# Kernel tuning notes

Measured on AMD Instinct MI355X. Metric: run time of the kernel, lower is better.

The kernel has to match this reference:

```python
import jax, jax.numpy as jnp
import numpy as np

MARGIN = 0.3


def setup_inputs() -> dict:
    key = jax.random.key(0)
    k1, k2 = jax.random.split(key)
    B, D, NCLS = 4096, 2048, 64
    inputs = jax.random.normal(k1, (B, D), dtype=jnp.float32)
    targets = jax.random.randint(k2, (B,), 0, NCLS, dtype=jnp.int64)
    return {"inputs": inputs, "targets": targets}


def _triplet_loss(inputs, targets, margin):
    sq = jnp.sum(inputs * inputs, axis=1)  # [B]
    distmat = sq[:, None] + sq[None, :] - 2.0 * (inputs @ inputs.T)  # [B, B]
    distmat = jnp.sqrt(jnp.clip(distmat, 1e-12, None))
    same = targets[None, :] == targets[:, None]  # [B, B]; includes diagonal
    neg_inf = jnp.float32(-jnp.inf)
    pos_inf = jnp.float32(jnp.inf)
    d_pos = jnp.max(jnp.where(same, distmat, neg_inf), axis=1)  # hardest positive
    d_neg = jnp.min(jnp.where(same, pos_inf, distmat), axis=1)  # hardest negative
    # MarginRankingLoss(x1=d_neg, x2=d_pos, y=1): mean(relu(-(d_neg - d_pos) + margin))
    return jnp.mean(jax.nn.relu(d_pos - d_neg + margin))


def reference(inputs, targets):
    return _triplet_loss(inputs, targets, MARGIN)
```

## Files before the change

kernel.cpp:

```cpp
#include <hip/hip_runtime.h>
#include <hip/hip_bf16.h>


typedef __attribute__((ext_vector_type(8))) short short8;
typedef __attribute__((ext_vector_type(4))) float f32x4;
using bf16 = __hip_bfloat16;

#define BN_ROWS 4096
#define D_DIM   2048
#define TILE    128
#define BK      64
#define MARGIN  0.3f

__device__ __forceinline__ void gload16(const bf16* g, bf16* l) {
  __builtin_amdgcn_global_load_lds(
      (const __attribute__((address_space(1))) void*)g,
      (__attribute__((address_space(3))) void*)l, 16, 0, 0);
}

__global__ __launch_bounds__(256) void prep_kernel(
    const float* __restrict__ x, bf16* __restrict__ xb, float* __restrict__ sqv,
    unsigned* __restrict__ pos, unsigned* __restrict__ neg) {
  const int row = blockIdx.x;
  const int t = threadIdx.x;
  const float4* xr = (const float4*)(x + (size_t)row * D_DIM) + (size_t)t * 2;
  float4 a = xr[0];
  float4 b = xr[1];
  float s = a.x * a.x + a.y * a.y + a.z * a.z + a.w * a.w +
            b.x * b.x + b.y * b.y + b.z * b.z + b.w * b.w;
  union { short8 v; bf16 h[8]; } u;
  u.h[0] = __float2bfloat16(a.x);
  u.h[1] = __float2bfloat16(a.y);
  u.h[2] = __float2bfloat16(a.z);
  u.h[3] = __float2bfloat16(a.w);
  u.h[4] = __float2bfloat16(b.x);
  u.h[5] = __float2bfloat16(b.y);
  u.h[6] = __float2bfloat16(b.z);
  u.h[7] = __float2bfloat16(b.w);
  *(short8*)(xb + (size_t)row * D_DIM + (size_t)t * 8) = u.v;

  #pragma unroll
  for (int o = 32; o; o >>= 1) s += __shfl_down(s, o, 64);
  __shared__ float red[4];
  if ((t & 63) == 0) red[t >> 6] = s;
  __syncthreads();
  if (t == 0) {
    sqv[row] = red[0] + red[1] + red[2] + red[3];
    pos[row] = 0u;
    neg[row] = 0x7F800000u;
  }
}

__global__ __launch_bounds__(256) void gram_kernel(
    const bf16* __restrict__ xb, const float* __restrict__ sqv,
    const int* __restrict__ tgt, unsigned* __restrict__ pos,
    unsigned* __restrict__ neg) {
  __shared__ bf16 As[TILE * BK];
  __shared__ bf16 Bs[TILE * BK];
  const int t = threadIdx.x;
  const int wave = t >> 6, lane = t & 63;
  const int rowBase = blockIdx.y * TILE;
  const int colBase = blockIdx.x * TILE;
  const int wr = wave >> 1, wc = wave & 1;
  const int lhi = lane >> 4, llo = lane & 15;

  f32x4 acc[4][4];
  #pragma unroll
  for (int m = 0; m < 4; ++m)
    #pragma unroll
    for (int n = 0; n < 4; ++n) acc[m][n] = (f32x4){0.f, 0.f, 0.f, 0.f};

  const int srow = lane >> 3;
  const int swz = (lane & 7) ^ srow;

  for (int k0 = 0; k0 < D_DIM; k0 += BK) {
    #pragma unroll
    for (int c = 0; c < 4; ++c) {
      const int chunk = wave * 4 + c;
      const size_t kcol = (size_t)k0 + (size_t)swz * 8;
      gload16(xb + (size_t)(rowBase + chunk * 8 + srow) * D_DIM + kcol,
              As + chunk * 512);
      gload16(xb + (size_t)(colBase + chunk * 8 + srow) * D_DIM + kcol,
              Bs + chunk * 512);
    }
    asm volatile("s_waitcnt vmcnt(0)" ::: "memory");
    __syncthreads();

    #pragma unroll
    for (int kk = 0; kk < 2; ++kk) {
      short8 af[4], bfr[4];
      #pragma unroll
      for (int m = 0; m < 4; ++m) {
        const int row = wr * 64 + m * 16 + llo;
        const int c16 = (kk * 4 + lhi) ^ (row & 7);
        af[m] = *(const short8*)(As + row * 64 + c16 * 8);
      }
      #pragma unroll
      for (int n = 0; n < 4; ++n) {
        const int row = wc * 64 + n * 16 + llo;
        const int c16 = (kk * 4 + lhi) ^ (row & 7);
        bfr[n] = *(const short8*)(Bs + row * 64 + c16 * 8);
      }
      #pragma unroll
      for (int m = 0; m < 4; ++m)
        #pragma unroll
        for (int n = 0; n < 4; ++n)
          acc[m][n] = __builtin_amdgcn_mfma_f32_16x16x32_bf16(
              af[m], bfr[n], acc[m][n], 0, 0, 0);
    }
    __syncthreads();
  }

  float sqj[4];
  int tgj[4];
  #pragma unroll
  for (int n = 0; n < 4; ++n) {
    const int j = colBase + wc * 64 + n * 16 + llo;
    sqj[n] = sqv[j];
    tgj[n] = tgt[j];
  }
  #pragma unroll
  for (int m = 0; m < 4; ++m) {
    #pragma unroll
    for (int r = 0; r < 4; ++r) {
      const int i = rowBase + wr * 64 + m * 16 + lhi * 4 + r;
      const float sqi = sqv[i];
      const int tgi = tgt[i];
      float pm = 0.0f;
      float nm = __uint_as_float(0x7F800000u);
      #pragma unroll
      for (int n = 0; n < 4; ++n) {
        const float g = acc[m][n][r];
        const float d2 = sqi + sqj[n] - 2.0f * g;
        const float d = sqrtf(fmaxf(d2, 1e-12f));
        if (tgj[n] == tgi) pm = fmaxf(pm, d);
        else               nm = fminf(nm, d);
      }
      #pragma unroll
      for (int o = 1; o < 16; o <<= 1) {
        pm = fmaxf(pm, __shfl_xor(pm, o, 64));
        nm = fminf(nm, __shfl_xor(nm, o, 64));
      }
      if (llo == 0) {
        atomicMax(pos + i, __float_as_uint(pm));
        atomicMin(neg + i, __float_as_uint(nm));
      }
    }
  }
}

__global__ __launch_bounds__(1024) void loss_kernel(
    const unsigned* __restrict__ pos, const unsigned* __restrict__ neg,
    float* __restrict__ out) {
  const int t = threadIdx.x;
  float s = 0.f;
  for (int i = t; i < BN_ROWS; i += 1024) {
    const float dp = __uint_as_float(pos[i]);
    const float dn = __uint_as_float(neg[i]);
    const float v = dp - dn + MARGIN;
    s += v > 0.f ? v : 0.f;
  }
  #pragma unroll
  for (int o = 32; o; o >>= 1) s += __shfl_down(s, o, 64);
  __shared__ float red[16];
  if ((t & 63) == 0) red[t >> 6] = s;
  __syncthreads();
  if (t < 16) {
    float v = red[t];
    #pragma unroll
    for (int o = 8; o; o >>= 1) v += __shfl_down(v, o, 16);
    if (t == 0) out[0] = v * (1.0f / (float)BN_ROWS);
  }
}

extern "C" void kernel_launch(void* const* d_in, const int* in_sizes, int n_in,
                              void* d_out, int out_size, void* d_ws, size_t ws_size,
                              hipStream_t stream) {
  const float* x = (const float*)d_in[0];
  const int* tgt = (const int*)d_in[1];
  float* out = (float*)d_out;

  char* ws = (char*)d_ws;
  bf16* xb = (bf16*)ws;
  float* sqv = (float*)(ws + (size_t)BN_ROWS * D_DIM * 2);
  unsigned* pos = (unsigned*)((char*)sqv + BN_ROWS * 4);
  unsigned* neg = (unsigned*)((char*)pos + BN_ROWS * 4);

  prep_kernel<<<BN_ROWS, 256, 0, stream>>>(x, xb, sqv, pos, neg);
  gram_kernel<<<dim3(BN_ROWS / TILE, BN_ROWS / TILE), 256, 0, stream>>>(
      xb, sqv, tgt, pos, neg);
  loss_kernel<<<1, 1024, 0, stream>>>(pos, neg, out);
}
```

Measured before the change: 173.2 us.

## Exploit Gram matrix symmetry by computing only upper-triangular tiles

The gram kernel now launches only the upper-triangular 128x128 tiles, mapping a linear block id to (row, col) tile indices. Each tile reduces its distances both per row and per column, with atomics on both, so the mirrored tile is never computed. This roughly halves the MFMA and load work but adds column reductions, extra atomics and index math. The prep kernel also switches to coalesced float4 loads with 8-byte bf16 stores.

New measurement: 173.3 us. About the same (+0.1%).

```diff
diff --git a/kernel.cpp b/kernel.cpp
--- a/kernel.cpp
+++ b/kernel.cpp
@@ -10,6 +10,8 @@
 #define D_DIM   2048
 #define TILE    128
 #define BK      64
+#define NB      (BN_ROWS / TILE)
+#define NBLK    (NB * (NB + 1) / 2)
 #define MARGIN  0.3f
 
 __device__ __forceinline__ void gload16(const bf16* g, bf16* l) {
@@ -23,22 +25,21 @@
     unsigned* __restrict__ pos, unsigned* __restrict__ neg) {
   const int row = blockIdx.x;
   const int t = threadIdx.x;
-  const float4* xr = (const float4*)(x + (size_t)row * D_DIM) + (size_t)t * 2;
-  float4 a = xr[0];
-  float4 b = xr[1];
-  float s = a.x * a.x + a.y * a.y + a.z * a.z + a.w * a.w +
-            b.x * b.x + b.y * b.y + b.z * b.z + b.w * b.w;
-  union { short8 v; bf16 h[8]; } u;
-  u.h[0] = __float2bfloat16(a.x);
-  u.h[1] = __float2bfloat16(a.y);
-  u.h[2] = __float2bfloat16(a.z);
-  u.h[3] = __float2bfloat16(a.w);
-  u.h[4] = __float2bfloat16(b.x);
-  u.h[5] = __float2bfloat16(b.y);
-  u.h[6] = __float2bfloat16(b.z);
-  u.h[7] = __float2bfloat16(b.w);
-  *(short8*)(xb + (size_t)row * D_DIM + (size_t)t * 8) = u.v;
-
+  const float4* xr = (const float4*)(x + (size_t)row * D_DIM);
+  bf16* xbr = xb + (size_t)row * D_DIM;
+  float s = 0.f;
+  #pragma unroll
+  for (int p = 0; p < 2; ++p) {
+    const int idx = t + p * 256;
+    float4 a = xr[idx];
+    s += a.x * a.x + a.y * a.y + a.z * a.z + a.w * a.w;
+    union { ushort4 v; bf16 h[4]; } u;
+    u.h[0] = __float2bfloat16(a.x);
+    u.h[1] = __float2bfloat16(a.y);
+    u.h[2] = __float2bfloat16(a.z);
+    u.h[3] = __float2bfloat16(a.w);
+    *(ushort4*)(xbr + (size_t)idx * 4) = u.v;
+  }
   #pragma unroll
   for (int o = 32; o; o >>= 1) s += __shfl_down(s, o, 64);
   __shared__ float red[4];
@@ -59,8 +60,15 @@
   __shared__ bf16 Bs[TILE * BK];
   const int t = threadIdx.x;
   const int wave = t >> 6, lane = t & 63;
-  const int rowBase = blockIdx.y * TILE;
-  const int colBase = blockIdx.x * TILE;
+
+  const int id = blockIdx.x;
+  int by = (int)(0.5f * (65.0f - sqrtf(4225.0f - 8.0f * (float)id)));
+  while (by * NB - (by * (by - 1)) / 2 > id) --by;
+  while ((by + 1) * NB - ((by + 1) * by) / 2 <= id) ++by;
+  const int bx = by + (id - (by * NB - (by * (by - 1)) / 2));
+  const int rowBase = by * TILE;
+  const int colBase = bx * TILE;
+
   const int wr = wave >> 1, wc = wave & 1;
   const int lhi = lane >> 4, llo = lane & 15;
 
@@ -111,6 +119,7 @@
     __syncthreads();
   }
 
+  const float inf = __uint_as_float(0x7F800000u);
   float sqj[4];
   int tgj[4];
   #pragma unroll
@@ -119,6 +128,9 @@
     sqj[n] = sqv[j];
     tgj[n] = tgt[j];
   }
+  float colP[4] = {0.f, 0.f, 0.f, 0.f};
+  float colN[4] = {inf, inf, inf, inf};
+
   #pragma unroll
   for (int m = 0; m < 4; ++m) {
     #pragma unroll
@@ -126,15 +138,19 @@
       const int i = rowBase + wr * 64 + m * 16 + lhi * 4 + r;
       const float sqi = sqv[i];
       const int tgi = tgt[i];
-      float pm = 0.0f;
-      float nm = __uint_as_float(0x7F800000u);
+      float pm = 0.0f, nm = inf;
       #pragma unroll
       for (int n = 0; n < 4; ++n) {
         const float g = acc[m][n][r];
         const float d2 = sqi + sqj[n] - 2.0f * g;
         const float d = sqrtf(fmaxf(d2, 1e-12f));
-        if (tgj[n] == tgi) pm = fmaxf(pm, d);
-        else               nm = fminf(nm, d);
+        if (tgj[n] == tgi) {
+          pm = fmaxf(pm, d);
+          colP[n] = fmaxf(colP[n], d);
+        } else {
+          nm = fminf(nm, d);
+          colN[n] = fminf(colN[n], d);
+        }
       }
       #pragma unroll
       for (int o = 1; o < 16; o <<= 1) {
@@ -145,6 +161,19 @@
         atomicMax(pos + i, __float_as_uint(pm));
         atomicMin(neg + i, __float_as_uint(nm));
       }
+    }
+  }
+  #pragma unroll
+  for (int n = 0; n < 4; ++n) {
+    float cp = colP[n], cn = colN[n];
+    cp = fmaxf(cp, __shfl_xor(cp, 16, 64));
+    cp = fmaxf(cp, __shfl_xor(cp, 32, 64));
+    cn = fminf(cn, __shfl_xor(cn, 16, 64));
+    cn = fminf(cn, __shfl_xor(cn, 32, 64));
+    if (lane < 16) {
+      const int j = colBase + wc * 64 + n * 16 + llo;
+      atomicMax(pos + j, __float_as_uint(cp));
+      atomicMin(neg + j, __float_as_uint(cn));
     }
   }
 }
@@ -187,7 +216,6 @@
   unsigned* neg = (unsigned*)((char*)pos + BN_ROWS * 4);
 
   prep_kernel<<<BN_ROWS, 256, 0, stream>>>(x, xb, sqv, pos, neg);
-  gram_kernel<<<dim3(BN_ROWS / TILE, BN_ROWS / TILE), 256, 0, stream>>>(
-      xb, sqv, tgt, pos, neg);
+  gram_kernel<<<NBLK, 256, 0, stream>>>(xb, sqv, tgt, pos, neg);
   loss_kernel<<<1, 1024, 0, stream>>>(pos, neg, out);
 }
```
